# Kernel optimization log

Hardware: AMD Instinct MI355X
Metric: run time of the kernel (lower is better)

The kernel has to match this reference:

```python
import jax, jax.numpy as jnp
import numpy as np

D_MODEL, D_STATE, D_CONV, EXPAND, L = 512, 16, 4, 2, 2048
D_INNER = EXPAND * D_MODEL


def _dwconv_causal(x, w, b):
    # x: (L, D), w: (D, K), b: (D,). torch Conv1d(groups=D, padding=K-1)[..., :L]
    K = w.shape[1]
    xp = jnp.pad(x, ((K - 1, 0), (0, 0)))
    windows = jnp.stack([xp[k:k + x.shape[0]] for k in range(K)], axis=-1)  # (L, D, K)
    return jnp.einsum('ldk,dk->ld', windows, w) + b


def _ssm_dir(x, inW, inb, cw, cb, xpW, xpb, dtW, dtb, outW, outb, A_log, Dp):
    xz = x @ inW + inb                      # (L, 2*Di)
    x_ssm, z = xz[:, :D_INNER], xz[:, D_INNER:]
    x_ssm = _dwconv_causal(x_ssm, cw, cb)   # (L, Di)
    sp = jax.nn.silu(x_ssm) @ xpW + xpb     # (L, Di + 2*S)
    delta = sp[:, :D_INNER]
    B = sp[:, D_INNER:D_INNER + D_STATE]
    C = sp[:, D_INNER + D_STATE:]
    dt = jax.nn.softplus(delta @ dtW + dtb)  # (L, Di)
    A = -jnp.exp(A_log)                      # (Di, S)
    dA = jnp.exp(dt[:, :, None] * A[None])                      # (L, Di, S)
    dBu = dt[:, :, None] * B[:, None, :] * x_ssm[:, :, None]    # (L, Di, S)

    def step(h, inp):
        a, bu = inp
        h = a * h + bu
        return h, h

    h0 = jnp.zeros((D_INNER, D_STATE), x.dtype)
    _, hs = jax.lax.scan(step, h0, (dA, dBu))   # (L, Di, S)
    y = jnp.einsum('lds,ls->ld', hs, C) + Dp * x_ssm
    return (y * jax.nn.silu(z)) @ outW + outb


def _make_params(key):
    ks = jax.random.split(key, 32)
    i = iter(range(32))
    def w(shape, scale=0.02):
        return (jax.random.normal(ks[next(i)], shape, jnp.float32) * scale)
    p = {}
    for pre in ('fwd_', 'bwd_'):
        p[pre + 'in_W'] = w((D_MODEL, 2 * D_INNER))
        p[pre + 'in_b'] = w((2 * D_INNER,))
        p[pre + 'conv_w'] = w((D_INNER, D_CONV), 0.1)
        p[pre + 'conv_b'] = w((D_INNER,))
        p[pre + 'xp_W'] = w((D_INNER, D_INNER + 2 * D_STATE))
        p[pre + 'xp_b'] = w((D_INNER + 2 * D_STATE,))
        p[pre + 'dt_W'] = w((D_INNER, D_INNER))
        p[pre + 'dt_b'] = w((D_INNER,))
        p[pre + 'out_W'] = w((D_INNER, D_MODEL))
        p[pre + 'out_b'] = w((D_MODEL,))
    p['A_log'] = jax.random.normal(ks[next(i)], (D_INNER, D_STATE), jnp.float32) * 0.5
    p['D_param'] = jnp.ones((D_INNER,), jnp.float32)
    p['fusion_W'] = w((2 * D_MODEL, D_MODEL))
    p['fusion_b'] = w((D_MODEL,))
    return p


def setup_inputs() -> dict:
    key = jax.random.key(0)
    kx, kp = jax.random.split(key)
    inp = {'x': jax.random.normal(kx, (L, D_MODEL), jnp.float32)}
    inp.update(_make_params(kp))
    return inp


def reference(x,
              fwd_in_W, fwd_in_b, fwd_conv_w, fwd_conv_b, fwd_xp_W, fwd_xp_b,
              fwd_dt_W, fwd_dt_b, fwd_out_W, fwd_out_b,
              bwd_in_W, bwd_in_b, bwd_conv_w, bwd_conv_b, bwd_xp_W, bwd_xp_b,
              bwd_dt_W, bwd_dt_b, bwd_out_W, bwd_out_b,
              A_log, D_param, fusion_W, fusion_b):
    out_fwd = _ssm_dir(x, fwd_in_W, fwd_in_b, fwd_conv_w, fwd_conv_b,
                       fwd_xp_W, fwd_xp_b, fwd_dt_W, fwd_dt_b,
                       fwd_out_W, fwd_out_b, A_log, D_param)
    out_bwd = _ssm_dir(x[::-1], bwd_in_W, bwd_in_b, bwd_conv_w, bwd_conv_b,
                       bwd_xp_W, bwd_xp_b, bwd_dt_W, bwd_dt_b,
                       bwd_out_W, bwd_out_b, A_log, D_param)[::-1]
    return jnp.concatenate([out_fwd, out_bwd], axis=-1) @ fusion_W + fusion_b
```

## Files before the change

kernel.cpp:

```cpp
#include <hip/hip_runtime.h>
#include <cmath>

#define L_SEQ 2048
#define DM 512
#define DI 1024
#define DS 16
#define NSP 1056
#define NC 64
#define CL 32

typedef unsigned short ushortT;
typedef unsigned int u32;
typedef __attribute__((ext_vector_type(8))) short short8;
typedef __attribute__((ext_vector_type(4))) float float4_t;
typedef __attribute__((address_space(1))) u32 gu32;
typedef __attribute__((address_space(3))) u32 lu32;

__device__ __forceinline__ float sigm(float x) { return 1.0f / (1.0f + __expf(-x)); }

__device__ __forceinline__ ushortT f2bf(float f) {
    unsigned u = __float_as_uint(f);
    unsigned r = u + 0x7FFFu + ((u >> 16) & 1u);
    return (ushortT)(r >> 16);
}

__device__ __forceinline__ void gl2lds16(const ushortT* g, ushortT* l) {
    __builtin_amdgcn_global_load_lds((gu32*)g, (lu32*)l, 16, 0, 0);
}

struct WC {
    const float* src[11];
    ushortT* dst[11];
    int ss[11], soff[11], ds_[11], tN[11], mode[11];
    int off[12];
};

__global__ __launch_bounds__(256) void prep_all(
    WC wc, int nW,
    const float* __restrict__ x, ushortT* __restrict__ xb,
    const float* __restrict__ xpb0, const float* __restrict__ xpb1,
    const float* __restrict__ dtW0, const float* __restrict__ dtW1,
    const float* __restrict__ dtb0, const float* __restrict__ dtb1,
    const float* __restrict__ outb0, const float* __restrict__ outb1,
    const float* __restrict__ fuW, const float* __restrict__ fub,
    float* __restrict__ BFdt0, float* __restrict__ BFdt1, float* __restrict__ BFof)
{
    __shared__ ushortT t[32][33];
    __shared__ float red[256];
    int b = blockIdx.x;
    int tid = threadIdx.x;
    if (b < nW) {
        int m = 0;
        while (b >= wc.off[m + 1]) ++m;
        int tl = b - wc.off[m];
        int n0 = (tl % wc.tN[m]) * 32;
        int k0 = (tl / wc.tN[m]) * 32;
        const float* W = wc.src[m];
        ushortT* D = wc.dst[m];
        int ss = wc.ss[m], soff = wc.soff[m], ds = wc.ds_[m];
        int tx = tid & 31, ty = tid >> 5;
        if (wc.mode[m] == 1) {
            #pragma unroll
            for (int i = 0; i < 32; i += 8)
                D[(size_t)(k0 + ty + i) * ds + n0 + tx] =
                    f2bf(W[(size_t)(k0 + ty + i) * ss + soff + n0 + tx]);
        } else {
            #pragma unroll
            for (int i = 0; i < 32; i += 8)
                t[ty + i][tx] = f2bf(W[(size_t)(k0 + ty + i) * ss + soff + n0 + tx]);
            __syncthreads();
            #pragma unroll
            for (int i = 0; i < 32; i += 8)
                D[(size_t)(n0 + ty + i) * ds + k0 + tx] = t[tx][ty + i];
        }
        return;
    }
    b -= nW;
    if (b < 1024) {
        int i = (b * 256 + tid) * 4;
        float4_t v = *(const float4_t*)(x + i);
        xb[i + 0] = f2bf(v[0]); xb[i + 1] = f2bf(v[1]);
        xb[i + 2] = f2bf(v[2]); xb[i + 3] = f2bf(v[3]);
        return;
    }
    int o = b - 1024;
    float acc = 0.0f;
    if (o < 2112) {
        int dir = o >= 1056;
        int m = o - dir * 1056;
        const float* xpb = dir ? xpb1 : xpb0;
        float* BF = dir ? BFdt1 : BFdt0;
        if (m >= 1024) {
            if (tid == 0) BF[m] = xpb[m];
            return;
        }
        const float* dtW = dir ? dtW1 : dtW0;
        const float* dtb = dir ? dtb1 : dtb0;
        for (int n = tid; n < 1024; n += 256) acc += xpb[n] * dtW[n * 1024 + m];
        red[tid] = acc;
        __syncthreads();
        for (int s = 128; s > 0; s >>= 1) {
            if (tid < s) red[tid] += red[tid + s];
            __syncthreads();
        }
        if (tid == 0) BF[m] = red[0] + dtb[m];
    } else {
        int n = o - 2112;
        for (int j = tid; j < 1024; j += 256) {
            float ob = (j < 512) ? outb0[j] : outb1[j - 512];
            acc += ob * fuW[(size_t)j * 512 + n];
        }
        red[tid] = acc;
        __syncthreads();
        for (int s = 128; s > 0; s >>= 1) {
            if (tid < s) red[tid] += red[tid + s];
            __syncthreads();
        }
        if (tid == 0) BFof[n] = red[0] + fub[n];
    }
}

template<int BM, int BN>
__device__ __forceinline__ void gemm_core(
    ushortT* As, ushortT* Bs,
    const ushortT* __restrict__ A, int lda, int revA,
    const ushortT* __restrict__ A2, int dualK,
    const ushortT* __restrict__ W,
    const float* __restrict__ bias,
    float* __restrict__ Cf, int ldcf,
    float* __restrict__ Cf2, int ldcf2, int Nsplit,
    ushortT* __restrict__ Cb, int ldcb,
    int M, int N, int K, int epi)
{
    constexpr int BK = 64;
    constexpr int MI = BM / 32;
    constexpr int NI = BN / 32;
    constexpr int CA = BM / 32;
    constexpr int CB = BN / 32;
    constexpr int ABUF = BM * BK;
    constexpr int BBUF = BN * BK;

    const int tid  = threadIdx.x;
    const int wave = tid >> 6;
    const int lane = tid & 63;
    const int quad = lane >> 4;
    const int r    = lane & 15;
    const int wm   = (wave >> 1) * (BM / 2);
    const int wn   = (wave & 1) * (BN / 2);
    const int bm   = blockIdx.y * BM;
    const int bn   = blockIdx.x * BN;

    const int lrow = lane >> 3;
    const int lk   = ((lane & 7) ^ lrow) * 8;

    const ushortT* gA[CA]; const ushortT* gA2[CA]; ushortT* lA[CA];
    #pragma unroll
    for (int c = 0; c < CA; ++c) {
        int row = bm + c * 32 + wave * 8 + lrow;
        int r0 = revA ? (M - 1 - row) : row;
        gA[c] = A + (size_t)r0 * lda + lk;
        gA2[c] = dualK ? (A2 + (size_t)(M - 1 - row) * lda + lk) : gA[c];
        lA[c] = &As[(c * 32 + wave * 8) * BK];
    }
    const ushortT* gB[CB]; ushortT* lB[CB];
    #pragma unroll
    for (int c = 0; c < CB; ++c) {
        int row = bn + c * 32 + wave * 8 + lrow;
        if (row > N - 1) row = N - 1;
        gB[c] = W + (size_t)row * K + lk;
        lB[c] = &Bs[(c * 32 + wave * 8) * BK];
    }

    float4_t acc[MI][NI];
    #pragma unroll
    for (int i = 0; i < MI; ++i)
        #pragma unroll
        for (int j = 0; j < NI; ++j)
            acc[i][j] = (float4_t){0.f, 0.f, 0.f, 0.f};

    const int nsteps = K >> 6;

    auto stage = [&](int step, int buf) {
        int kq = step << 6;
        #pragma unroll
        for (int c = 0; c < CA; ++c) {
            const ushortT* s = (!dualK || kq < 1024) ? gA[c] + kq : gA2[c] + (kq - 1024);
            gl2lds16(s, lA[c] + buf * ABUF);
        }
        #pragma unroll
        for (int c = 0; c < CB; ++c)
            gl2lds16(gB[c] + kq, lB[c] + buf * BBUF);
    };
    auto compute = [&](int buf) {
        #pragma unroll
        for (int kh = 0; kh < 2; ++kh) {
            const int slot = (((kh * 4 + quad) ^ (lane & 7)) * 8);
            short8 af[MI], bf[NI];
            #pragma unroll
            for (int mi = 0; mi < MI; ++mi)
                af[mi] = *(const short8*)&As[buf * ABUF + (wm + mi * 16 + r) * BK + slot];
            #pragma unroll
            for (int ni = 0; ni < NI; ++ni)
                bf[ni] = *(const short8*)&Bs[buf * BBUF + (wn + ni * 16 + r) * BK + slot];
            #pragma unroll
            for (int mi = 0; mi < MI; ++mi)
                #pragma unroll
                for (int ni = 0; ni < NI; ++ni)
                    acc[mi][ni] = __builtin_amdgcn_mfma_f32_16x16x32_bf16(
                        af[mi], bf[ni], acc[mi][ni], 0, 0, 0);
        }
    };

    stage(0, 0);
    for (int i = 0; i < nsteps; i += 2) {
        __syncthreads();
        if (i + 1 < nsteps) stage(i + 1, 1);
        compute(0);
        __syncthreads();
        if (i + 2 < nsteps) stage(i + 2, 0);
        compute(1);
    }

    #pragma unroll
    for (int mi = 0; mi < MI; ++mi) {
        int rowb = bm + wm + mi * 16 + quad * 4;
        #pragma unroll
        for (int ni = 0; ni < NI; ++ni) {
            int gn = bn + wn + ni * 16 + r;
            if (gn < N) {
                float bv = bias ? bias[gn] : 0.0f;
                #pragma unroll
                for (int j = 0; j < 4; ++j) {
                    int orow = rowb + j;
                    float v = acc[mi][ni][j] + bv;
                    if (epi == 1 && gn < Nsplit) v = (v > 20.0f) ? v : log1pf(__expf(v));
                    if (gn < Nsplit) {
                        if (Cf) Cf[(size_t)orow * ldcf + gn] = v;
                    } else if (Cf2) {
                        Cf2[(size_t)orow * ldcf2 + gn - Nsplit] = v;
                    }
                    if (Cb) Cb[(size_t)orow * ldcb + gn] = f2bf(v);
                }
            }
        }
    }
}

template<int BM, int BN>
__global__ __launch_bounds__(256) void gemm_bf16(
    const ushortT* __restrict__ A, int lda, long long Astr, int revAmode,
    const ushortT* __restrict__ W, long long Wstr,
    const float* __restrict__ bias0, const float* __restrict__ bias1,
    float* __restrict__ Cf, int ldcf, long long Cfstr,
    float* __restrict__ Cf2, int ldcf2, long long Cf2str, int Nsplit,
    int M, int N, int K, int epi)
{
    __shared__ ushortT As[2 * BM * 64];
    __shared__ ushortT Bs[2 * BN * 64];
    const int dir = blockIdx.z;
    const ushortT* Ad = A;
    const ushortT* A2 = A;
    int revA = 0, dualK = 0;
    if (revAmode == 3) { dualK = 1; A2 = A + Astr; }
    else { Ad += (size_t)dir * Astr; revA = (revAmode == 2) ? dir : revAmode; }
    gemm_core<BM, BN>(As, Bs,
        Ad, lda, revA, A2, dualK,
        W + (size_t)dir * Wstr,
        dir ? bias1 : bias0,
        Cf ? Cf + (size_t)dir * Cfstr : nullptr, ldcf,
        Cf2 ? Cf2 + (size_t)dir * Cf2str : nullptr, ldcf2, Nsplit,
        nullptr, 0, M, N, K, epi);
}

__global__ __launch_bounds__(256) void gemm_fold(
    const ushortT* __restrict__ WtDt, const ushortT* __restrict__ XpD,
    ushortT* __restrict__ WtXpF,
    const ushortT* __restrict__ WtFu, const ushortT* __restrict__ OutC,
    ushortT* __restrict__ WtOF2)
{
    __shared__ ushortT As[2 * 64 * 64];
    __shared__ ushortT Bs[2 * 64 * 64];
    int z = blockIdx.z;
    if (z < 2) {
        gemm_core<64, 64>(As, Bs,
            WtDt + (size_t)z * DI * DI, DI, 0, nullptr, 0,
            XpD + (size_t)z * DI * DI,
            nullptr, nullptr, 0, nullptr, 0, DI,
            WtXpF + (size_t)z * NSP * DI, DI,
            DI, DI, DI, 0);
    } else {
        if (blockIdx.y >= 8) return;
        int d = z - 2;
        gemm_core<64, 64>(As, Bs,
            WtFu + (size_t)d * DM, DI, 0, nullptr, 0,
            OutC + (size_t)d * DI * DM,
            nullptr, nullptr, 0, nullptr, 0, DI,
            WtOF2 + (size_t)d * DI, 2 * DI,
            DM, DI, DM, 0);
    }
}

__global__ __launch_bounds__(256) void conv_k(
    const float* __restrict__ XZ,
    const float* __restrict__ cw0, const float* __restrict__ cw1,
    const float* __restrict__ cb0, const float* __restrict__ cb1,
    float* __restrict__ XC, ushortT* __restrict__ SCb)
{
    int dir = blockIdx.z;
    XZ += (size_t)dir * L_SEQ * 2 * DI;
    XC += (size_t)dir * L_SEQ * DI;
    SCb += (size_t)dir * L_SEQ * DI;
    const float* cw = dir ? cw1 : cw0;
    const float* cb = dir ? cb1 : cb0;
    int idx = blockIdx.x * 256 + threadIdx.x;
    int d = idx & (DI - 1);
    int l = idx >> 10;
    float w0 = cw[d * 4 + 0], w1 = cw[d * 4 + 1], w2 = cw[d * 4 + 2], w3 = cw[d * 4 + 3];
    float acc = cb[d];
    if (l >= 3) acc += XZ[(size_t)(l - 3) * (2 * DI) + d] * w0;
    if (l >= 2) acc += XZ[(size_t)(l - 2) * (2 * DI) + d] * w1;
    if (l >= 1) acc += XZ[(size_t)(l - 1) * (2 * DI) + d] * w2;
    acc += XZ[(size_t)l * (2 * DI) + d] * w3;
    XC[idx] = acc;
    SCb[idx] = f2bf(acc * sigm(acc));
}

__global__ __launch_bounds__(256) void scanA_k(
    const float* __restrict__ DT, const float* __restrict__ XC,
    const float* __restrict__ BC, const float* __restrict__ Alog,
    float* __restrict__ Pend, float* __restrict__ Hl)
{
    __shared__ float Bsh[CL][DS];
    int dir = blockIdx.z;
    int c = blockIdx.y;
    int d = blockIdx.x * 256 + threadIdx.x;
    DT += (size_t)dir * L_SEQ * DI;
    XC += (size_t)dir * L_SEQ * DI;
    BC += (size_t)dir * L_SEQ * 32;
    int l0 = c * CL;
    for (int i = threadIdx.x; i < CL * DS; i += 256) {
        int ll = i >> 4, ss = i & 15;
        Bsh[ll][ss] = BC[(size_t)(l0 + ll) * 32 + ss];
    }
    __syncthreads();
    float Ae[DS], h[DS], P[DS];
    #pragma unroll
    for (int s = 0; s < DS; ++s) { Ae[s] = -__expf(Alog[d * DS + s]); h[s] = 0.f; P[s] = 1.f; }
    for (int t = 0; t < CL; ++t) {
        int l = l0 + t;
        float dt = DT[(size_t)l * DI + d];
        float xv = XC[(size_t)l * DI + d];
        float dtx = dt * xv;
        #pragma unroll
        for (int s = 0; s < DS; ++s) {
            float e = __expf(dt * Ae[s]);
            h[s] = e * h[s] + dtx * Bsh[t][s];
            P[s] *= e;
        }
    }
    size_t o = ((size_t)(dir * NC + c) * DI + d) * DS;
    #pragma unroll
    for (int s = 0; s < DS; ++s) { Pend[o + s] = P[s]; Hl[o + s] = h[s]; }
}

__global__ __launch_bounds__(256) void scanB_k(
    const float* __restrict__ Pend, const float* __restrict__ Hl, float* __restrict__ Hs)
{
    int idx = blockIdx.x * 256 + threadIdx.x;
    float h = 0.f;
    int ds = idx & 16383;
    int dir = idx >> 14;
    for (int c = 0; c < NC; ++c) {
        size_t o = ((size_t)(dir * NC + c)) * (DI * DS) + ds;
        Hs[o] = h;
        h = Pend[o] * h + Hl[o];
    }
}

__global__ __launch_bounds__(256) void scanC_k(
    const float* __restrict__ DT, const float* __restrict__ XC,
    const float* __restrict__ BC, const float* __restrict__ XZ,
    const float* __restrict__ Alog, const float* __restrict__ Dp,
    const float* __restrict__ Hs, ushortT* __restrict__ Gb)
{
    __shared__ float Bsh[CL][DS];
    __shared__ float Csh[CL][DS];
    int dir = blockIdx.z;
    int c = blockIdx.y;
    int d = blockIdx.x * 256 + threadIdx.x;
    DT += (size_t)dir * L_SEQ * DI;
    XC += (size_t)dir * L_SEQ * DI;
    BC += (size_t)dir * L_SEQ * 32;
    XZ += (size_t)dir * L_SEQ * (2 * DI);
    Gb += (size_t)dir * L_SEQ * DI;
    int l0 = c * CL;
    for (int i = threadIdx.x; i < CL * DS; i += 256) {
        int ll = i >> 4, ss = i & 15;
        size_t base = (size_t)(l0 + ll) * 32;
        Bsh[ll][ss] = BC[base + ss];
        Csh[ll][ss] = BC[base + DS + ss];
    }
    __syncthreads();
    float Ae[DS], h[DS];
    size_t o = ((size_t)(dir * NC + c) * DI + d) * DS;
    #pragma unroll
    for (int s = 0; s < DS; ++s) { Ae[s] = -__expf(Alog[d * DS + s]); h[s] = Hs[o + s]; }
    float dpv = Dp[d];
    for (int t = 0; t < CL; ++t) {
        int l = l0 + t;
        float dt = DT[(size_t)l * DI + d];
        float xv = XC[(size_t)l * DI + d];
        float dtx = dt * xv;
        float y = 0.f;
        #pragma unroll
        for (int s = 0; s < DS; ++s) {
            float e = __expf(dt * Ae[s]);
            h[s] = e * h[s] + dtx * Bsh[t][s];
            y += h[s] * Csh[t][s];
        }
        y += dpv * xv;
        float z = XZ[(size_t)l * (2 * DI) + DI + d];
        Gb[(size_t)l * DI + d] = f2bf(y * (z * sigm(z)));
    }
}

extern "C" void kernel_launch(void* const* d_in, const int* in_sizes, int n_in,
                              void* d_out, int out_size, void* d_ws, size_t ws_size,
                              hipStream_t stream)
{
    (void)in_sizes; (void)n_in; (void)out_size; (void)ws_size;
    const float* x = (const float*)d_in[0];
    const float* inW[2]  = {(const float*)d_in[1],  (const float*)d_in[11]};
    const float* inb[2]  = {(const float*)d_in[2],  (const float*)d_in[12]};
    const float* cw[2]   = {(const float*)d_in[3],  (const float*)d_in[13]};
    const float* cb[2]   = {(const float*)d_in[4],  (const float*)d_in[14]};
    const float* xpW[2]  = {(const float*)d_in[5],  (const float*)d_in[15]};
    const float* xpb[2]  = {(const float*)d_in[6],  (const float*)d_in[16]};
    const float* dtW[2]  = {(const float*)d_in[7],  (const float*)d_in[17]};
    const float* dtb[2]  = {(const float*)d_in[8],  (const float*)d_in[18]};
    const float* outW[2] = {(const float*)d_in[9],  (const float*)d_in[19]};
    const float* outb[2] = {(const float*)d_in[10], (const float*)d_in[20]};
    const float* Alog = (const float*)d_in[21];
    const float* Dp   = (const float*)d_in[22];
    const float* fuW  = (const float*)d_in[23];
    const float* fub  = (const float*)d_in[24];
    float* out = (float*)d_out;

    float* ws = (float*)d_ws;
    size_t off = 0;
    auto alloc = [&](size_t n) { float* p = ws + off; off += n; return p; };
    float* XZ   = alloc((size_t)2 * L_SEQ * 2 * DI);
    float* XC   = alloc((size_t)2 * L_SEQ * DI);
    float* DTb  = alloc((size_t)2 * L_SEQ * DI);
    float* BCf  = alloc((size_t)2 * L_SEQ * 32);
    float* Pend = alloc((size_t)2 * NC * DI * DS);
    float* Hl   = alloc((size_t)2 * NC * DI * DS);
    float* Hs   = alloc((size_t)2 * NC * DI * DS);
    float* BFdt0 = alloc(1056);
    float* BFdt1 = alloc(1056);
    float* BFof  = alloc(512);

    ushortT* wsu = (ushortT*)(ws + off);
    size_t uoff = 0;
    auto ualloc = [&](size_t n) { ushortT* p = wsu + uoff; uoff += n; return p; };
    ushortT* WtIn  = ualloc((size_t)2 * (2 * DI) * DM);
    ushortT* WtDt  = ualloc((size_t)2 * DI * DI);
    ushortT* WtFu  = ualloc((size_t)DM * DI);
    ushortT* WtXpF = ualloc((size_t)2 * NSP * DI);
    ushortT* XpD   = ualloc((size_t)2 * DI * DI);
    ushortT* OutC  = ualloc((size_t)2 * DI * DM);
    ushortT* WtOF2 = ualloc((size_t)DM * 2 * DI);
    ushortT* XB    = ualloc((size_t)L_SEQ * DM);
    ushortT* SCb   = ualloc((size_t)2 * L_SEQ * DI);
    ushortT* Gb    = ualloc((size_t)2 * L_SEQ * DI);

    dim3 blk(256);

    WC wc;
    struct E { const float* s; ushortT* d; int ss, so, ds, N, K, mode; };
    E es[11] = {
        {inW[0],  WtIn,                          2 * DI, 0,    DM, 2 * DI, DM, 0},
        {inW[1],  WtIn + (size_t)2 * DI * DM,    2 * DI, 0,    DM, 2 * DI, DM, 0},
        {dtW[0],  WtDt,                          DI,     0,    DI, DI,     DI, 0},
        {dtW[1],  WtDt + (size_t)DI * DI,        DI,     0,    DI, DI,     DI, 0},
        {fuW,     WtFu,                          DM,     0,    DI, DM,     DI, 0},
        {xpW[0],  WtXpF + (size_t)DI * DI,       NSP,    DI,   DI, 32,     DI, 0},
        {xpW[1],  WtXpF + (size_t)NSP * DI + (size_t)DI * DI, NSP, DI, DI, 32, DI, 0},
        {xpW[0],  XpD,                           NSP,    0,    DI, DI,     DI, 1},
        {xpW[1],  XpD + (size_t)DI * DI,         NSP,    0,    DI, DI,     DI, 1},
        {outW[0], OutC,                          DM,     0,    DM, DM,     DI, 1},
        {outW[1], OutC + (size_t)DI * DM,        DM,     0,    DM, DM,     DI, 1},
    };
    wc.off[0] = 0;
    for (int m = 0; m < 11; ++m) {
        wc.src[m] = es[m].s; wc.dst[m] = es[m].d;
        wc.ss[m] = es[m].ss; wc.soff[m] = es[m].so; wc.ds_[m] = es[m].ds;
        wc.tN[m] = es[m].N / 32; wc.mode[m] = es[m].mode;
        wc.off[m + 1] = wc.off[m] + (es[m].N / 32) * (es[m].K / 32);
    }
    int nW = wc.off[11];
    prep_all<<<dim3(nW + 1024 + 2624), blk, 0, stream>>>(
        wc, nW, x, XB,
        xpb[0], xpb[1], dtW[0], dtW[1], dtb[0], dtb[1],
        outb[0], outb[1], fuW, fub, BFdt0, BFdt1, BFof);

    gemm_fold<<<dim3(16, 16, 4), blk, 0, stream>>>(WtDt, XpD, WtXpF, WtFu, OutC, WtOF2);

    gemm_bf16<128, 64><<<dim3(32, 16, 2), blk, 0, stream>>>(
        XB, DM, 0, 2, WtIn, (long long)2 * DI * DM, inb[0], inb[1],
        XZ, 2 * DI, (long long)L_SEQ * 2 * DI, nullptr, 0, 0, 2 * DI,
        L_SEQ, 2 * DI, DM, 0);
    conv_k<<<dim3(L_SEQ * DI / 256, 1, 2), blk, 0, stream>>>(
        XZ, cw[0], cw[1], cb[0], cb[1], XC, SCb);
    gemm_bf16<128, 64><<<dim3((NSP + 63) / 64, 16, 2), blk, 0, stream>>>(
        SCb, DI, (long long)L_SEQ * DI, 0, WtXpF, (long long)NSP * DI, BFdt0, BFdt1,
        DTb, DI, (long long)L_SEQ * DI, BCf, 32, (long long)L_SEQ * 32, DI,
        L_SEQ, NSP, DI, 1);
    scanA_k<<<dim3(DI / 256, NC, 2), blk, 0, stream>>>(DTb, XC, BCf, Alog, Pend, Hl);
    scanB_k<<<dim3(2 * DI * DS / 256), blk, 0, stream>>>(Pend, Hl, Hs);
    scanC_k<<<dim3(DI / 256, NC, 2), blk, 0, stream>>>(DTb, XC, BCf, XZ, Alog, Dp, Hs, Gb);
    gemm_bf16<64, 64><<<dim3(DM / 64, 32, 1), blk, 0, stream>>>(
        Gb, DI, (long long)L_SEQ * DI, 3, WtOF2, 0, BFof, BFof,
        out, DM, 0, nullptr, 0, 0, DM,
        L_SEQ, DM, 2 * DI, 0);
}
```

Before: 326.2 us.

## Store intermediates in bf16, recompute conv in scans, swizzle GEMM block order

```diff
diff --git a/kernel.cpp b/kernel.cpp
--- a/kernel.cpp
+++ b/kernel.cpp
@@ -22,6 +22,9 @@
     unsigned u = __float_as_uint(f);
     unsigned r = u + 0x7FFFu + ((u >> 16) & 1u);
     return (ushortT)(r >> 16);
+}
+__device__ __forceinline__ float b2f(ushortT u) {
+    return __uint_as_float(((u32)u) << 16);
 }
 
 __device__ __forceinline__ void gl2lds16(const ushortT* g, ushortT* l) {
@@ -122,7 +125,7 @@
 
 template<int BM, int BN>
 __device__ __forceinline__ void gemm_core(
-    ushortT* As, ushortT* Bs,
+    ushortT* As, ushortT* Bs, int bm, int bn,
     const ushortT* __restrict__ A, int lda, int revA,
     const ushortT* __restrict__ A2, int dualK,
     const ushortT* __restrict__ W,
@@ -130,6 +133,7 @@
     float* __restrict__ Cf, int ldcf,
     float* __restrict__ Cf2, int ldcf2, int Nsplit,
     ushortT* __restrict__ Cb, int ldcb,
+    ushortT* __restrict__ Cb2, int ldcb2,
     int M, int N, int K, int epi)
 {
     constexpr int BK = 64;
@@ -147,8 +151,6 @@
     const int r    = lane & 15;
     const int wm   = (wave >> 1) * (BM / 2);
     const int wn   = (wave & 1) * (BN / 2);
-    const int bm   = blockIdx.y * BM;
-    const int bn   = blockIdx.x * BN;
 
     const int lrow = lane >> 3;
     const int lk   = ((lane & 7) ^ lrow) * 8;
@@ -233,13 +235,14 @@
                 for (int j = 0; j < 4; ++j) {
                     int orow = rowb + j;
                     float v = acc[mi][ni][j] + bv;
-                    if (epi == 1 && gn < Nsplit) v = (v > 20.0f) ? v : log1pf(__expf(v));
                     if (gn < Nsplit) {
+                        if (epi == 1) v = (v > 20.0f) ? v : log1pf(__expf(v));
                         if (Cf) Cf[(size_t)orow * ldcf + gn] = v;
-                    } else if (Cf2) {
-                        Cf2[(size_t)orow * ldcf2 + gn - Nsplit] = v;
+                        if (Cb) Cb[(size_t)orow * ldcb + gn] = f2bf(v);
+                    } else {
+                        if (Cf2) Cf2[(size_t)orow * ldcf2 + gn - Nsplit] = v;
+                        if (Cb2) Cb2[(size_t)orow * ldcb2 + gn - Nsplit] = f2bf(v);
                     }
-                    if (Cb) Cb[(size_t)orow * ldcb + gn] = f2bf(v);
                 }
             }
         }
@@ -253,23 +256,42 @@
     const float* __restrict__ bias0, const float* __restrict__ bias1,
     float* __restrict__ Cf, int ldcf, long long Cfstr,
     float* __restrict__ Cf2, int ldcf2, long long Cf2str, int Nsplit,
-    int M, int N, int K, int epi)
+    ushortT* __restrict__ Cb, int ldcb, long long Cbstr,
+    ushortT* __restrict__ Cb2, int ldcb2, long long Cb2str,
+    int swz, int M, int N, int K, int epi)
 {
     __shared__ ushortT As[2 * BM * 64];
     __shared__ ushortT Bs[2 * BN * 64];
-    const int dir = blockIdx.z;
+    int bx = blockIdx.x, by = blockIdx.y, dir = blockIdx.z;
+    if (swz) {
+        int gx = gridDim.x, gy = gridDim.y, gz = gridDim.z;
+        long long b = ((long long)dir * gy + by) * gx + bx;
+        int xc = (int)(b & 7);
+        long long k = b >> 3;
+        if (gz == 2) {
+            dir = xc & 1;
+            int q = xc >> 1;
+            if (swz == 1) { int qc = gx >> 2; bx = q * qc + (int)(k % qc); by = (int)(k / qc); }
+            else          { int qc = gy >> 2; by = q * qc + (int)(k % qc); bx = (int)(k / qc); }
+        } else {
+            if (swz == 1) { int qc = gx >> 3; bx = xc * qc + (int)(k % qc); by = (int)(k / qc); }
+            else          { int qc = gy >> 3; by = xc * qc + (int)(k % qc); bx = (int)(k / qc); }
+        }
+    }
     const ushortT* Ad = A;
     const ushortT* A2 = A;
     int revA = 0, dualK = 0;
     if (revAmode == 3) { dualK = 1; A2 = A + Astr; }
     else { Ad += (size_t)dir * Astr; revA = (revAmode == 2) ? dir : revAmode; }
-    gemm_core<BM, BN>(As, Bs,
+    gemm_core<BM, BN>(As, Bs, by * BM, bx * BN,
         Ad, lda, revA, A2, dualK,
         W + (size_t)dir * Wstr,
         dir ? bias1 : bias0,
         Cf ? Cf + (size_t)dir * Cfstr : nullptr, ldcf,
         Cf2 ? Cf2 + (size_t)dir * Cf2str : nullptr, ldcf2, Nsplit,
-        nullptr, 0, M, N, K, epi);
+        Cb ? Cb + (size_t)dir * Cbstr : nullptr, ldcb,
+        Cb2 ? Cb2 + (size_t)dir * Cb2str : nullptr, ldcb2,
+        M, N, K, epi);
 }
 
 __global__ __launch_bounds__(256) void gemm_fold(
@@ -282,33 +304,32 @@
     __shared__ ushortT Bs[2 * 64 * 64];
     int z = blockIdx.z;
     if (z < 2) {
-        gemm_core<64, 64>(As, Bs,
+        gemm_core<64, 64>(As, Bs, blockIdx.y * 64, blockIdx.x * 64,
             WtDt + (size_t)z * DI * DI, DI, 0, nullptr, 0,
             XpD + (size_t)z * DI * DI,
             nullptr, nullptr, 0, nullptr, 0, DI,
-            WtXpF + (size_t)z * NSP * DI, DI,
+            WtXpF + (size_t)z * NSP * DI, DI, nullptr, 0,
             DI, DI, DI, 0);
     } else {
         if (blockIdx.y >= 8) return;
         int d = z - 2;
-        gemm_core<64, 64>(As, Bs,
+        gemm_core<64, 64>(As, Bs, blockIdx.y * 64, blockIdx.x * 64,
             WtFu + (size_t)d * DM, DI, 0, nullptr, 0,
             OutC + (size_t)d * DI * DM,
             nullptr, nullptr, 0, nullptr, 0, DI,
-            WtOF2 + (size_t)d * DI, 2 * DI,
+            WtOF2 + (size_t)d * DI, 2 * DI, nullptr, 0,
             DM, DI, DM, 0);
     }
 }
 
 __global__ __launch_bounds__(256) void conv_k(
-    const float* __restrict__ XZ,
+    const ushortT* __restrict__ XSb,
     const float* __restrict__ cw0, const float* __restrict__ cw1,
     const float* __restrict__ cb0, const float* __restrict__ cb1,
-    float* __restrict__ XC, ushortT* __restrict__ SCb)
+    ushortT* __restrict__ SCb)
 {
     int dir = blockIdx.z;
-    XZ += (size_t)dir * L_SEQ * 2 * DI;
-    XC += (size_t)dir * L_SEQ * DI;
+    XSb += (size_t)dir * L_SEQ * DI;
     SCb += (size_t)dir * L_SEQ * DI;
     const float* cw = dir ? cw1 : cw0;
     const float* cb = dir ? cb1 : cb0;
@@ -317,39 +338,49 @@
     int l = idx >> 10;
     float w0 = cw[d * 4 + 0], w1 = cw[d * 4 + 1], w2 = cw[d * 4 + 2], w3 = cw[d * 4 + 3];
     float acc = cb[d];
-    if (l >= 3) acc += XZ[(size_t)(l - 3) * (2 * DI) + d] * w0;
-    if (l >= 2) acc += XZ[(size_t)(l - 2) * (2 * DI) + d] * w1;
-    if (l >= 1) acc += XZ[(size_t)(l - 1) * (2 * DI) + d] * w2;
-    acc += XZ[(size_t)l * (2 * DI) + d] * w3;
-    XC[idx] = acc;
+    if (l >= 3) acc += b2f(XSb[(size_t)(l - 3) * DI + d]) * w0;
+    if (l >= 2) acc += b2f(XSb[(size_t)(l - 2) * DI + d]) * w1;
+    if (l >= 1) acc += b2f(XSb[(size_t)(l - 1) * DI + d]) * w2;
+    acc += b2f(XSb[(size_t)l * DI + d]) * w3;
     SCb[idx] = f2bf(acc * sigm(acc));
 }
 
 __global__ __launch_bounds__(256) void scanA_k(
-    const float* __restrict__ DT, const float* __restrict__ XC,
+    const ushortT* __restrict__ DTb, const ushortT* __restrict__ XSb,
     const float* __restrict__ BC, const float* __restrict__ Alog,
+    const float* __restrict__ cw0, const float* __restrict__ cw1,
+    const float* __restrict__ cb0, const float* __restrict__ cb1,
     float* __restrict__ Pend, float* __restrict__ Hl)
 {
     __shared__ float Bsh[CL][DS];
     int dir = blockIdx.z;
     int c = blockIdx.y;
     int d = blockIdx.x * 256 + threadIdx.x;
-    DT += (size_t)dir * L_SEQ * DI;
-    XC += (size_t)dir * L_SEQ * DI;
-    BC += (size_t)dir * L_SEQ * 32;
+    DTb += (size_t)dir * L_SEQ * DI;
+    XSb += (size_t)dir * L_SEQ * DI;
+    BC  += (size_t)dir * L_SEQ * 32;
+    const float* cw = dir ? cw1 : cw0;
+    const float* cb = dir ? cb1 : cb0;
     int l0 = c * CL;
     for (int i = threadIdx.x; i < CL * DS; i += 256) {
         int ll = i >> 4, ss = i & 15;
         Bsh[ll][ss] = BC[(size_t)(l0 + ll) * 32 + ss];
     }
     __syncthreads();
+    float w0 = cw[d * 4 + 0], w1 = cw[d * 4 + 1], w2 = cw[d * 4 + 2], w3 = cw[d * 4 + 3];
+    float cbv = cb[d];
+    float x3 = (l0 >= 3) ? b2f(XSb[(size_t)(l0 - 3) * DI + d]) : 0.f;
+    float x2 = (l0 >= 2) ? b2f(XSb[(size_t)(l0 - 2) * DI + d]) : 0.f;
+    float x1 = (l0 >= 1) ? b2f(XSb[(size_t)(l0 - 1) * DI + d]) : 0.f;
     float Ae[DS], h[DS], P[DS];
     #pragma unroll
     for (int s = 0; s < DS; ++s) { Ae[s] = -__expf(Alog[d * DS + s]); h[s] = 0.f; P[s] = 1.f; }
     for (int t = 0; t < CL; ++t) {
         int l = l0 + t;
-        float dt = DT[(size_t)l * DI + d];
-        float xv = XC[(size_t)l * DI + d];
+        float x0 = b2f(XSb[(size_t)l * DI + d]);
+        float xv = cbv + w0 * x3 + w1 * x2 + w2 * x1 + w3 * x0;
+        x3 = x2; x2 = x1; x1 = x0;
+        float dt = b2f(DTb[(size_t)l * DI + d]);
         float dtx = dt * xv;
         #pragma unroll
         for (int s = 0; s < DS; ++s) {
@@ -378,9 +409,11 @@
 }
 
 __global__ __launch_bounds__(256) void scanC_k(
-    const float* __restrict__ DT, const float* __restrict__ XC,
-    const float* __restrict__ BC, const float* __restrict__ XZ,
+    const ushortT* __restrict__ DTb, const ushortT* __restrict__ XSb,
+    const float* __restrict__ BC, const ushortT* __restrict__ Zb,
     const float* __restrict__ Alog, const float* __restrict__ Dp,
+    const float* __restrict__ cw0, const float* __restrict__ cw1,
+    const float* __restrict__ cb0, const float* __restrict__ cb1,
     const float* __restrict__ Hs, ushortT* __restrict__ Gb)
 {
     __shared__ float Bsh[CL][DS];
@@ -388,11 +421,13 @@
     int dir = blockIdx.z;
     int c = blockIdx.y;
     int d = blockIdx.x * 256 + threadIdx.x;
-    DT += (size_t)dir * L_SEQ * DI;
-    XC += (size_t)dir * L_SEQ * DI;
-    BC += (size_t)dir * L_SEQ * 32;
-    XZ += (size_t)dir * L_SEQ * (2 * DI);
-    Gb += (size_t)dir * L_SEQ * DI;
+    DTb += (size_t)dir * L_SEQ * DI;
+    XSb += (size_t)dir * L_SEQ * DI;
+    BC  += (size_t)dir * L_SEQ * 32;
+    Zb  += (size_t)dir * L_SEQ * DI;
+    Gb  += (size_t)dir * L_SEQ * DI;
+    const float* cw = dir ? cw1 : cw0;
+    const float* cb = dir ? cb1 : cb0;
     int l0 = c * CL;
     for (int i = threadIdx.x; i < CL * DS; i += 256) {
         int ll = i >> 4, ss = i & 15;
@@ -401,6 +436,11 @@
         Csh[ll][ss] = BC[base + DS + ss];
     }
     __syncthreads();
+    float w0 = cw[d * 4 + 0], w1 = cw[d * 4 + 1], w2 = cw[d * 4 + 2], w3 = cw[d * 4 + 3];
+    float cbv = cb[d];
+    float x3 = (l0 >= 3) ? b2f(XSb[(size_t)(l0 - 3) * DI + d]) : 0.f;
+    float x2 = (l0 >= 2) ? b2f(XSb[(size_t)(l0 - 2) * DI + d]) : 0.f;
+    float x1 = (l0 >= 1) ? b2f(XSb[(size_t)(l0 - 1) * DI + d]) : 0.f;
     float Ae[DS], h[DS];
     size_t o = ((size_t)(dir * NC + c) * DI + d) * DS;
     #pragma unroll
@@ -408,8 +448,10 @@
     float dpv = Dp[d];
     for (int t = 0; t < CL; ++t) {
         int l = l0 + t;
-        float dt = DT[(size_t)l * DI + d];
-        float xv = XC[(size_t)l * DI + d];
+        float x0 = b2f(XSb[(size_t)l * DI + d]);
+        float xv = cbv + w0 * x3 + w1 * x2 + w2 * x1 + w3 * x0;
+        x3 = x2; x2 = x1; x1 = x0;
+        float dt = b2f(DTb[(size_t)l * DI + d]);
         float dtx = dt * xv;
         float y = 0.f;
         #pragma unroll
@@ -419,7 +461,7 @@
             y += h[s] * Csh[t][s];
         }
         y += dpv * xv;
-        float z = XZ[(size_t)l * (2 * DI) + DI + d];
+        float z = b2f(Zb[(size_t)l * DI + d]);
         Gb[(size_t)l * DI + d] = f2bf(y * (z * sigm(z)));
     }
 }
@@ -449,9 +491,6 @@
     float* ws = (float*)d_ws;
     size_t off = 0;
     auto alloc = [&](size_t n) { float* p = ws + off; off += n; return p; };
-    float* XZ   = alloc((size_t)2 * L_SEQ * 2 * DI);
-    float* XC   = alloc((size_t)2 * L_SEQ * DI);
-    float* DTb  = alloc((size_t)2 * L_SEQ * DI);
     float* BCf  = alloc((size_t)2 * L_SEQ * 32);
     float* Pend = alloc((size_t)2 * NC * DI * DS);
     float* Hl   = alloc((size_t)2 * NC * DI * DS);
@@ -471,7 +510,10 @@
     ushortT* OutC  = ualloc((size_t)2 * DI * DM);
     ushortT* WtOF2 = ualloc((size_t)DM * 2 * DI);
     ushortT* XB    = ualloc((size_t)L_SEQ * DM);
+    ushortT* XSb   = ualloc((size_t)2 * L_SEQ * DI);
+    ushortT* Zb    = ualloc((size_t)2 * L_SEQ * DI);
     ushortT* SCb   = ualloc((size_t)2 * L_SEQ * DI);
+    ushortT* DTbB  = ualloc((size_t)2 * L_SEQ * DI);
     ushortT* Gb    = ualloc((size_t)2 * L_SEQ * DI);
 
     dim3 blk(256);
@@ -508,19 +550,24 @@
 
     gemm_bf16<128, 64><<<dim3(32, 16, 2), blk, 0, stream>>>(
         XB, DM, 0, 2, WtIn, (long long)2 * DI * DM, inb[0], inb[1],
-        XZ, 2 * DI, (long long)L_SEQ * 2 * DI, nullptr, 0, 0, 2 * DI,
-        L_SEQ, 2 * DI, DM, 0);
+        nullptr, 0, 0, nullptr, 0, 0, DI,
+        XSb, DI, (long long)L_SEQ * DI, Zb, DI, (long long)L_SEQ * DI,
+        1, L_SEQ, 2 * DI, DM, 0);
     conv_k<<<dim3(L_SEQ * DI / 256, 1, 2), blk, 0, stream>>>(
-        XZ, cw[0], cw[1], cb[0], cb[1], XC, SCb);
+        XSb, cw[0], cw[1], cb[0], cb[1], SCb);
     gemm_bf16<128, 64><<<dim3((NSP + 63) / 64, 16, 2), blk, 0, stream>>>(
         SCb, DI, (long long)L_SEQ * DI, 0, WtXpF, (long long)NSP * DI, BFdt0, BFdt1,
-        DTb, DI, (long long)L_SEQ * DI, BCf, 32, (long long)L_SEQ * 32, DI,
-        L_SEQ, NSP, DI, 1);
-    scanA_k<<<dim3(DI / 256, NC, 2), blk, 0, stream>>>(DTb, XC, BCf, Alog, Pend, Hl);
+        nullptr, 0, 0, BCf, 32, (long long)L_SEQ * 32, DI,
+        DTbB, DI, (long long)L_SEQ * DI, nullptr, 0, 0,
+        2, L_SEQ, NSP, DI, 1);
+    scanA_k<<<dim3(DI / 256, NC, 2), blk, 0, stream>>>(
+        DTbB, XSb, BCf, Alog, cw[0], cw[1], cb[0], cb[1], Pend, Hl);
     scanB_k<<<dim3(2 * DI * DS / 256), blk, 0, stream>>>(Pend, Hl, Hs);
-    scanC_k<<<dim3(DI / 256, NC, 2), blk, 0, stream>>>(DTb, XC, BCf, XZ, Alog, Dp, Hs, Gb);
+    scanC_k<<<dim3(DI / 256, NC, 2), blk, 0, stream>>>(
+        DTbB, XSb, BCf, Zb, Alog, Dp, cw[0], cw[1], cb[0], cb[1], Hs, Gb);
     gemm_bf16<64, 64><<<dim3(DM / 64, 32, 1), blk, 0, stream>>>(
         Gb, DI, (long long)L_SEQ * DI, 3, WtOF2, 0, BFof, BFof,
         out, DM, 0, nullptr, 0, 0, DM,
-        L_SEQ, DM, 2 * DI, 0);
-}
+        nullptr, 0, 0, nullptr, 0, 0,
+        2, L_SEQ, DM, 2 * DI, 0);
+}
```

Measured after the change: 326.3 us. Within noise of the previous version (+0.0%).
